# Kernel tuning notes

Measured on AMD Instinct MI355X. Metric: run time of the kernel, lower is better.

Reference implementation:

```python
import jax, jax.numpy as jnp
import numpy as np

M_QAM = 16
LEAD_SYMBOLS = 20000  # pilot prefix in 'test' mode
NSYMB = 40000
NMODES = 256


def qam_constellation(M):
    # square M-QAM grid, normalized to unit average energy (constellation / sqrt(Es))
    m = int(np.sqrt(M))
    levels = 2 * np.arange(m) - (m - 1)
    c = (levels[:, None] + 1j * levels[None, :]).ravel()
    Es = np.mean(np.abs(c) ** 2)
    return (c / np.sqrt(Es)).astype(np.complex64)  # [M]


def setup_inputs() -> dict:
    key = jax.random.key(0)
    k = jax.random.split(key, 4)
    return {
        "Ei_real": jax.random.normal(k[0], (NSYMB, NMODES), jnp.float32),
        "Ei_imag": jax.random.normal(k[1], (NSYMB, NMODES), jnp.float32),
        "tx_real": jax.random.normal(k[2], (NSYMB, NMODES), jnp.float32),
        "tx_imag": jax.random.normal(k[3], (NSYMB, NMODES), jnp.float32),
        "eta": jnp.full((1,), 0.1, jnp.float32),  # learnable 'ddpll eta' param
    }


def _ddpll(Ei, symbTx, Kv, constSymb, mode):
    # k0,k1,k2 = 2*tanh(arctanh(0.5)), 2*tanh(arctanh(-0.5)), 2*tanh(arctanh(0.5))
    k0, k1, k2 = 1.0, -1.0, 1.0

    def Lk(phi, y, target, m):
        z = y * jnp.exp(1j * phi)
        dec = jnp.min(jnp.abs(z - constSymb) ** 2)  # decision-directed (min over M points)
        pil = jnp.abs(z - target) ** 2              # pilot-aided
        return dec * m + pil * (1.0 - m)

    g = jax.vmap(jax.grad(Lk, argnums=0))  # per-mode d Lk / d phi

    def step(carry, data):
        u, phi = carry                 # u: [3, Nmodes], phi: [Nmodes]
        xk, yk, mk = data              # [Nmodes] each
        gk = g(phi, yk, xk, mk)
        u1 = u[2]                      # u[1] <- old u[2]
        u0 = k0 * u[0] + k1 * u1 + k2 * gk  # momentum filter output
        new_u = jnp.stack([u0, u1, gk])
        return (new_u, phi - Kv * u0), phi  # emit pre-update phase (phip)

    Nmodes = Ei.shape[1]
    carry0 = (jnp.zeros((3, Nmodes), jnp.float32), jnp.zeros((Nmodes,), jnp.float32))
    _, theta = jax.lax.scan(step, carry0, (symbTx, Ei, mode))
    theta = jnp.unwrap(theta, axis=0, period=np.pi / 2)
    return Ei * jnp.exp(1j * theta), theta


def reference(Ei_real, Ei_imag, tx_real, tx_imag, eta):
    Ei = Ei_real + 1j * Ei_imag          # [Nsymb, Nmodes] complex64
    symbTx = tx_real + 1j * tx_imag
    Kv = jnp.tanh(eta[0])                # lr = tanh(eta)
    # mode: 0 on pilot rows (first lead_symbols in 'test' mode), 1 elsewhere
    mode = jnp.ones((NSYMB, NMODES), jnp.float32).at[:LEAD_SYMBOLS].set(0.0)
    constSymb = jnp.asarray(qam_constellation(M_QAM))
    Eo, theta = _ddpll(Ei, symbTx, Kv, constSymb, mode)
    return jnp.stack([Eo.real, Eo.imag], axis=-1), theta  # [Nsymb, Nmodes, 2], [Nsymb, Nmodes]
```

## Files before the change

kernel.cpp:

```cpp
#include <hip/hip_runtime.h>
#include <math.h>

#define NSYMB  40000
#define NMODES 256
#define LEAD   20000
#define UF     8

static __device__ __forceinline__ float crhypotf(float a, float b) {
    const double da = (double)a, db = (double)b;
    return (float)sqrt(da * da + db * db);
}

static __device__ __forceinline__ float fmod_p2_exact(float xf) {
    const double y  = (double)1.57079632679489661923f;
    const double ry = 1.0 / ((double)1.57079632679489661923f);
    const double ax = fabs((double)xf);
    const double q  = __builtin_trunc(ax * ry);
    double r = __builtin_fma(-q, y, ax);
    r = (r < 0.0) ? (r + y) : ((r >= y) ? (r - y) : r);
    return copysignf((float)r, xf);
}

static __device__ __forceinline__ void cr_sincosf_nb(double x, float& sf, float& cf) {
    const double invpio2 = 6.36619772367581382433e-01;
    const double pio2_1  = 1.57079632673412561417e+00;
    const double pio2_1t = 6.07710050650619224932e-11;
    const double fn = __builtin_rint(x * invpio2);
    const double rr = __builtin_fma(-fn, pio2_1, x);
    const double yy = rr - fn * pio2_1t;
    const double z  = yy * yy;
    double ps = __builtin_fma(z, 1.58969099521155010221e-10, -2.50507602534068634195e-08);
    ps = __builtin_fma(z, ps,  2.75573137070700676789e-06);
    ps = __builtin_fma(z, ps, -1.98412698298579493134e-04);
    ps = __builtin_fma(z, ps,  8.33333333332248946124e-03);
    ps = __builtin_fma(z, ps, -1.66666666666666324348e-01);
    const double sv = __builtin_fma(yy * z, ps, yy);
    double pc = __builtin_fma(z, -1.13596475577881948265e-11, 2.08757232129817482790e-09);
    pc = __builtin_fma(z, pc, -2.75573143513906633035e-07);
    pc = __builtin_fma(z, pc,  2.48015872894767294178e-05);
    pc = __builtin_fma(z, pc, -1.38888888888741095749e-03);
    pc = __builtin_fma(z, pc,  4.16666666666666019037e-02);
    const double hz = 0.5 * z;
    const double w1 = 1.0 - hz;
    const double cv = w1 + (((1.0 - w1) - hz) + z * (z * pc));
    const int n = ((int)fn) & 3;
    const float S = (float)sv, C = (float)cv;
    const bool sw = (n & 1) != 0;
    const float sa = sw ? C : S;
    const float ca = sw ? S : C;
    sf = (n & 2) ? -sa : sa;
    cf = ((n + 1) & 2) ? -ca : ca;
}

static __device__ __attribute__((noinline)) float2 dd_slow(float zre, float zim) {
#pragma clang fp contract(off)
    const double s10 = sqrt(10.0);
    float Lf[4];
    Lf[0] = (float)(-3.0 / s10); Lf[1] = (float)(-1.0 / s10);
    Lf[2] = (float)( 1.0 / s10); Lf[3] = (float)( 3.0 / s10);
    float dv[16], rv[16], wres[16], wims[16];
    float dmin = __builtin_inff();
#pragma unroll
    for (int k = 0; k < 16; ++k) {
        const float wre = zre - Lf[k >> 2];
        const float wim = zim - Lf[k & 3];
        const float r = crhypotf(wre, wim);
        const float d = r * r;
        wres[k] = wre; wims[k] = wim; rv[k] = r; dv[k] = d;
        dmin = fminf(dmin, d);
    }
    int cnt = 0;
#pragma unroll
    for (int k = 0; k < 16; ++k) cnt += (dv[k] == dmin) ? 1 : 0;
    float A, B;
    if (cnt == 1) {
        int j = 0;
#pragma unroll
        for (int k = 0; k < 16; ++k) if (dv[k] == dmin) j = k;
        A = 2.0f * wres[j];
        B = -(2.0f * wims[j]);
    } else {
        const float ctd = 1.0f / (float)cnt;
        float sa = 0.0f, sb = 0.0f;
#pragma unroll
        for (int k = 0; k < 16; ++k) {
            if (dv[k] == dmin) {
                const float ctr  = (2.0f * rv[k]) * ctd;
                const float ctm2 = ctr / rv[k];
                sa += (ctm2 * wres[k]);
                sb += -(ctm2 * wims[k]);
            }
        }
        A = sa; B = sb;
    }
    return make_float2(A, B);
}

template<bool PILOT>
static __device__ __forceinline__ void phi_step(
    float yre, float yim, float txr, float txi,
    float Kv, const float* Lf, float& phi)
{
#pragma clang fp contract(off)
    const float QTHf = 0.63245553203367588f;
    float s, c;
    cr_sincosf_nb((double)phi, s, c);
    const float zre = (yre * c) - (yim * s);
    const float zim = (yre * s) + (yim * c);
    float A, B;
    if (PILOT) {
        const float wre = zre - txr;
        const float wim = zim - txi;
        A = 2.0f * wre;
        B = -(2.0f * wim);
    } else {
        const float tr = (zre < 0.0f) ? ((zre < -QTHf) ? Lf[0] : Lf[1])
                                      : ((zre <  QTHf) ? Lf[2] : Lf[3]);
        const float ti = (zim < 0.0f) ? ((zim < -QTHf) ? Lf[0] : Lf[1])
                                      : ((zim <  QTHf) ? Lf[2] : Lf[3]);
        const float wre0 = zre - tr;
        const float wim0 = zim - ti;
        A = 2.0f * wre0;
        B = -(2.0f * wim0);
        const float ar = fabsf(zre), ai = fabsf(zim);
        const float mr = fminf(fabsf(ar - QTHf), ar);
        const float mi = fminf(fabsf(ai - QTHf), ai);
        const bool slow = !(mr > 1e-4f && mi > 1e-4f);
        if (__builtin_expect(__ballot(slow) != 0ULL, 0)) {
            if (slow) { const float2 ab = dd_slow(zre, zim); A = ab.x; B = ab.y; }
        }
    }
    const float ct_e_re = (A * yre) - (B * yim);
    const float ct_e_im = (A * yim) + (B * yre);
    const float ct_v_im = (ct_e_re * s) + (ct_e_im * c);
    const float gk = -ct_v_im;
    phi = phi - (Kv * gk);
}

static __device__ __forceinline__ void unwrap_emit(
    int t, int m, float th, float& prev, float& cum, float* __restrict__ theta_out)
{
#pragma clang fp contract(off)
    const float P2f = 1.57079632679489661923f;
    const float P4f = 0.78539816339744830961f;
    const float dd = th - prev;
    float rm = fmod_p2_exact(dd + P4f);
    rm = (rm < 0.0f) ? rm + P2f : rm;
    float ddmod = rm - P4f;
    ddmod = (ddmod == -P4f && dd > 0.0f) ? P4f : ddmod;
    const bool take = (t > 0) && !(fabsf(dd) < P4f);
    cum = take ? cum + (ddmod - dd) : cum;
    prev = th;
    theta_out[t * NMODES + m] = th + cum;
}

__global__ __launch_bounds__(64)
void ddpll_seq(const float* __restrict__ ei_re,
               const float* __restrict__ ei_im,
               const float* __restrict__ tx_re,
               const float* __restrict__ tx_im,
               const float* __restrict__ eta,
               float* __restrict__ out)
{
#pragma clang fp contract(off)
    const int m = blockIdx.x * 64 + threadIdx.x;
    const float Kv = (float)tanh((double)eta[0]);

    const double s10 = sqrt(10.0);
    float Lf[4];
    Lf[0] = (float)(-3.0 / s10); Lf[1] = (float)(-1.0 / s10);
    Lf[2] = (float)( 1.0 / s10); Lf[3] = (float)( 3.0 / s10);

    float phi = 0.0f, prev = 0.0f, cum = 0.0f;
    float thb[UF];
    float* __restrict__ theta_out = out + (size_t)2 * NSYMB * NMODES;

    float pyr[UF], pyi[UF], pxr[UF], pxi[UF];
#pragma unroll
    for (int j = 0; j < UF; ++j) {
        const int idx = j * NMODES + m;
        pyr[j] = ei_re[idx]; pyi[j] = ei_im[idx];
        pxr[j] = tx_re[idx]; pxi[j] = tx_im[idx];
    }
    {
        float yr[UF], yi[UF], xr[UF], xi[UF];
#pragma unroll
        for (int j = 0; j < UF; ++j) { yr[j]=pyr[j]; yi[j]=pyi[j]; xr[j]=pxr[j]; xi[j]=pxi[j]; }
#pragma unroll
        for (int j = 0; j < UF; ++j) {
            const int idx = (UF + j) * NMODES + m;
            pyr[j] = ei_re[idx]; pyi[j] = ei_im[idx];
            pxr[j] = tx_re[idx]; pxi[j] = tx_im[idx];
        }
#pragma unroll
        for (int j = 0; j < UF; ++j) {
            thb[j] = phi;
            phi_step<true>(yr[j], yi[j], xr[j], xi[j], Kv, Lf, phi);
        }
    }
    for (int tb = UF; tb < LEAD; tb += UF) {
        float yr[UF], yi[UF], xr[UF], xi[UF];
#pragma unroll
        for (int j = 0; j < UF; ++j) { yr[j]=pyr[j]; yi[j]=pyi[j]; xr[j]=pxr[j]; xi[j]=pxi[j]; }
        const int nb = tb + UF;
#pragma unroll
        for (int j = 0; j < UF; ++j) {
            const int idx = (nb + j) * NMODES + m;
            pyr[j] = ei_re[idx]; pyi[j] = ei_im[idx];
            pxr[j] = tx_re[idx]; pxi[j] = tx_im[idx];
        }
#pragma unroll
        for (int j = 0; j < UF; ++j) {
            const float u = thb[j];
            thb[j] = phi;
            unwrap_emit(tb - UF + j, m, u, prev, cum, theta_out);
            phi_step<true>(yr[j], yi[j], xr[j], xi[j], Kv, Lf, phi);
        }
    }

#pragma unroll
    for (int j = 0; j < UF; ++j) {
        const int idx = (LEAD + j) * NMODES + m;
        pyr[j] = ei_re[idx]; pyi[j] = ei_im[idx];
    }
    for (int tb = LEAD; tb < NSYMB; tb += UF) {
        float yr[UF], yi[UF];
#pragma unroll
        for (int j = 0; j < UF; ++j) { yr[j]=pyr[j]; yi[j]=pyi[j]; }
        const int nb = tb + UF;
#pragma unroll
        for (int j = 0; j < UF; ++j) {
            const int tt = (nb + j < NSYMB) ? (nb + j) : (NSYMB - 1);
            const int idx = tt * NMODES + m;
            pyr[j] = ei_re[idx]; pyi[j] = ei_im[idx];
        }
#pragma unroll
        for (int j = 0; j < UF; ++j) {
            const float u = thb[j];
            thb[j] = phi;
            unwrap_emit(tb - UF + j, m, u, prev, cum, theta_out);
            phi_step<false>(yr[j], yi[j], 0.0f, 0.0f, Kv, Lf, phi);
        }
    }
#pragma unroll
    for (int j = 0; j < UF; ++j)
        unwrap_emit(NSYMB - UF + j, m, thb[j], prev, cum, theta_out);
}

__global__ __launch_bounds__(256)
void ddpll_rot(const float* __restrict__ ei_re,
               const float* __restrict__ ei_im,
               float* __restrict__ out)
{
    const int idx = blockIdx.x * 256 + threadIdx.x;
    const float U = out[(size_t)2 * NSYMB * NMODES + idx];
    float su, cu;
    sincosf(U, &su, &cu);
    const float yre = ei_re[idx], yim = ei_im[idx];
    out[2 * idx]     = (yre * cu) - (yim * su);
    out[2 * idx + 1] = (yre * su) + (yim * cu);
}

extern "C" void kernel_launch(void* const* d_in, const int* in_sizes, int n_in,
                              void* d_out, int out_size, void* d_ws, size_t ws_size,
                              hipStream_t stream)
{
    (void)in_sizes; (void)n_in; (void)out_size; (void)d_ws; (void)ws_size;
    const float* ei_re = (const float*)d_in[0];
    const float* ei_im = (const float*)d_in[1];
    ddpll_seq<<<dim3(NMODES / 64), dim3(64), 0, stream>>>(
        ei_re, ei_im,
        (const float*)d_in[2],
        (const float*)d_in[3],
        (const float*)d_in[4],
        (float*)d_out);
    ddpll_rot<<<dim3(NSYMB * NMODES / 256), dim3(256), 0, stream>>>(
        ei_re, ei_im, (float*)d_out);
}
```

Measured before the change: 12.93 ms.

## Split phase unwrap out of sequential PLL into parallel correction and scan kernels

The sequential per-mode PLL kernel now writes only the raw pre-update phase. Unwrapping is moved into a fully parallel kernel that computes per-step corrections into the Eo region of the output, used as scratch. A separate per-mode sequential kernel then prefix-sums those corrections. This takes the expensive double-precision fmod off the serial critical path, at the cost of two extra kernel launches and an extra round of global reads and writes.

```diff
diff --git a/kernel.cpp b/kernel.cpp
--- a/kernel.cpp
+++ b/kernel.cpp
@@ -137,23 +137,6 @@
     phi = phi - (Kv * gk);
 }
 
-static __device__ __forceinline__ void unwrap_emit(
-    int t, int m, float th, float& prev, float& cum, float* __restrict__ theta_out)
-{
-#pragma clang fp contract(off)
-    const float P2f = 1.57079632679489661923f;
-    const float P4f = 0.78539816339744830961f;
-    const float dd = th - prev;
-    float rm = fmod_p2_exact(dd + P4f);
-    rm = (rm < 0.0f) ? rm + P2f : rm;
-    float ddmod = rm - P4f;
-    ddmod = (ddmod == -P4f && dd > 0.0f) ? P4f : ddmod;
-    const bool take = (t > 0) && !(fabsf(dd) < P4f);
-    cum = take ? cum + (ddmod - dd) : cum;
-    prev = th;
-    theta_out[t * NMODES + m] = th + cum;
-}
-
 __global__ __launch_bounds__(64)
 void ddpll_seq(const float* __restrict__ ei_re,
                const float* __restrict__ ei_im,
@@ -171,9 +154,8 @@
     Lf[0] = (float)(-3.0 / s10); Lf[1] = (float)(-1.0 / s10);
     Lf[2] = (float)( 1.0 / s10); Lf[3] = (float)( 3.0 / s10);
 
-    float phi = 0.0f, prev = 0.0f, cum = 0.0f;
-    float thb[UF];
-    float* __restrict__ theta_out = out + (size_t)2 * NSYMB * NMODES;
+    float phi = 0.0f;
+    float* __restrict__ th_out = out + (size_t)2 * NSYMB * NMODES;
 
     float pyr[UF], pyi[UF], pxr[UF], pxi[UF];
 #pragma unroll
@@ -182,23 +164,7 @@
         pyr[j] = ei_re[idx]; pyi[j] = ei_im[idx];
         pxr[j] = tx_re[idx]; pxi[j] = tx_im[idx];
     }
-    {
-        float yr[UF], yi[UF], xr[UF], xi[UF];
-#pragma unroll
-        for (int j = 0; j < UF; ++j) { yr[j]=pyr[j]; yi[j]=pyi[j]; xr[j]=pxr[j]; xi[j]=pxi[j]; }
-#pragma unroll
-        for (int j = 0; j < UF; ++j) {
-            const int idx = (UF + j) * NMODES + m;
-            pyr[j] = ei_re[idx]; pyi[j] = ei_im[idx];
-            pxr[j] = tx_re[idx]; pxi[j] = tx_im[idx];
-        }
-#pragma unroll
-        for (int j = 0; j < UF; ++j) {
-            thb[j] = phi;
-            phi_step<true>(yr[j], yi[j], xr[j], xi[j], Kv, Lf, phi);
-        }
-    }
-    for (int tb = UF; tb < LEAD; tb += UF) {
+    for (int tb = 0; tb < LEAD; tb += UF) {
         float yr[UF], yi[UF], xr[UF], xi[UF];
 #pragma unroll
         for (int j = 0; j < UF; ++j) { yr[j]=pyr[j]; yi[j]=pyi[j]; xr[j]=pxr[j]; xi[j]=pxi[j]; }
@@ -211,9 +177,7 @@
         }
 #pragma unroll
         for (int j = 0; j < UF; ++j) {
-            const float u = thb[j];
-            thb[j] = phi;
-            unwrap_emit(tb - UF + j, m, u, prev, cum, theta_out);
+            th_out[(tb + j) * NMODES + m] = phi;
             phi_step<true>(yr[j], yi[j], xr[j], xi[j], Kv, Lf, phi);
         }
     }
@@ -236,15 +200,63 @@
         }
 #pragma unroll
         for (int j = 0; j < UF; ++j) {
-            const float u = thb[j];
-            thb[j] = phi;
-            unwrap_emit(tb - UF + j, m, u, prev, cum, theta_out);
+            th_out[(tb + j) * NMODES + m] = phi;
             phi_step<false>(yr[j], yi[j], 0.0f, 0.0f, Kv, Lf, phi);
         }
     }
-#pragma unroll
-    for (int j = 0; j < UF; ++j)
-        unwrap_emit(NSYMB - UF + j, m, thb[j], prev, cum, theta_out);
+}
+
+__global__ __launch_bounds__(256)
+void ddpll_unwrapc(const float* __restrict__ th, float* __restrict__ c)
+{
+#pragma clang fp contract(off)
+    const float P2f = 1.57079632679489661923f;
+    const float P4f = 0.78539816339744830961f;
+    const int idx = blockIdx.x * 256 + threadIdx.x;
+    float cv = 0.0f;
+    if (idx >= NMODES) {
+        const float thv  = th[idx];
+        const float prev = th[idx - NMODES];
+        const float dd = thv - prev;
+        float rm = fmod_p2_exact(dd + P4f);
+        rm = (rm < 0.0f) ? rm + P2f : rm;
+        float ddmod = rm - P4f;
+        ddmod = (ddmod == -P4f && dd > 0.0f) ? P4f : ddmod;
+        const bool take = !(fabsf(dd) < P4f);
+        cv = take ? (ddmod - dd) : 0.0f;
+    }
+    c[idx] = cv;
+}
+
+__global__ __launch_bounds__(64)
+void ddpll_scan(const float* __restrict__ c, float* __restrict__ th)
+{
+#pragma clang fp contract(off)
+    const int m = blockIdx.x * 64 + threadIdx.x;
+    float cum = 0.0f;
+    float pc_[UF], pt_[UF];
+#pragma unroll
+    for (int j = 0; j < UF; ++j) {
+        pc_[j] = c[j * NMODES + m];
+        pt_[j] = th[j * NMODES + m];
+    }
+    for (int tb = 0; tb < NSYMB; tb += UF) {
+        float cv[UF], tv[UF];
+#pragma unroll
+        for (int j = 0; j < UF; ++j) { cv[j]=pc_[j]; tv[j]=pt_[j]; }
+        const int nb = tb + UF;
+#pragma unroll
+        for (int j = 0; j < UF; ++j) {
+            const int tt = (nb + j < NSYMB) ? (nb + j) : (NSYMB - 1);
+            pc_[j] = c[tt * NMODES + m];
+            pt_[j] = th[tt * NMODES + m];
+        }
+#pragma unroll
+        for (int j = 0; j < UF; ++j) {
+            cum = cum + cv[j];
+            th[(tb + j) * NMODES + m] = tv[j] + cum;
+        }
+    }
 }
 
 __global__ __launch_bounds__(256)
@@ -268,12 +280,18 @@
     (void)in_sizes; (void)n_in; (void)out_size; (void)d_ws; (void)ws_size;
     const float* ei_re = (const float*)d_in[0];
     const float* ei_im = (const float*)d_in[1];
+    float* out = (float*)d_out;
+    float* th  = out + (size_t)2 * NSYMB * NMODES;
+    float* c   = out;
+
     ddpll_seq<<<dim3(NMODES / 64), dim3(64), 0, stream>>>(
         ei_re, ei_im,
         (const float*)d_in[2],
         (const float*)d_in[3],
         (const float*)d_in[4],
-        (float*)d_out);
+        out);
+    ddpll_unwrapc<<<dim3(NSYMB * NMODES / 256), dim3(256), 0, stream>>>(th, c);
+    ddpll_scan<<<dim3(NMODES / 64), dim3(64), 0, stream>>>(c, th);
     ddpll_rot<<<dim3(NSYMB * NMODES / 256), dim3(256), 0, stream>>>(
-        ei_re, ei_im, (float*)d_out);
-}
+        ei_re, ei_im, out);
+}
```

Measured after the change: 12.39 ms. 1.04x faster.
